# Optimization experiments

Measured on AMD Instinct MI355X. Metric: run time of the kernel, lower is better.

## Reference

```python
import jax, jax.numpy as jnp
import numpy as np
from jax import lax

K = 8  # diffusion channels
T = 3  # diffusion steps


def setup_inputs() -> dict:
    key = jax.random.key(0)
    k1, k2, k3 = jax.random.split(key, 3)
    x = jax.random.normal(k1, (16, 1, 512, 512), dtype=jnp.float32)
    # per-step conv weights [T, out=k, in=1, kh, kw] and biases [T, k]
    W = jax.random.normal(k2, (T, K, 1, 3, 3), dtype=jnp.float32) * 0.1
    b = jax.random.normal(k3, (T, K), dtype=jnp.float32) * 0.1
    return {"x": x, "W": W, "b": b}


def _g(d):
    # mode 1 edge-stopping function: exp(-|d| / (1 + d^2))
    return jnp.exp(-jnp.abs(d) / (1.0 + d * d))


def reference(x, W, b):
    in_x = x  # [N,1,H,W]
    for t in range(T):
        d1 = lax.conv_general_dilated(
            in_x, W[t], window_strides=(1, 1), padding="SAME",
            dimension_numbers=("NCHW", "OIHW", "NCHW"),
        ) + b[t][None, :, None, None]  # [N,K,H,W]
        features = _g(d1) * d1
        # squash_tensor: sum over the K channels, keep channel dim of 1
        in_x = in_x - jnp.sum(features, axis=1, keepdims=True) / K
    return in_x
```

## Files before the change

kernel.cpp:

```cpp
#include <hip/hip_runtime.h>

static constexpr int IMG  = 512;
static constexpr int TILE = 64;

template<int WR, int PS, bool TO_GLOBAL>
__device__ __forceinline__ void diffuse_step(
    const float* __restrict__ prev, float* __restrict__ cur,
    const float* __restrict__ Wt, const float* __restrict__ bt,
    int ty0, int tx0, int halo, int tid, float* __restrict__ gout)
{
    for (int idx = tid; idx < WR * WR; idx += 256) {
        const int r = idx / WR;
        const int c = idx - r * WR;
        const float* p = prev + r * PS + c;
        const float n0 = p[0],      n1 = p[1],      n2 = p[2];
        const float n3 = p[PS],     n4 = p[PS+1],   n5 = p[PS+2];
        const float n6 = p[2*PS],   n7 = p[2*PS+1], n8 = p[2*PS+2];
        float acc = 0.0f;
#pragma unroll
        for (int k = 0; k < 8; ++k) {
            const float* wk = Wt + 9 * k;
            float d = bt[k];
            d = fmaf(wk[0], n0, d);
            d = fmaf(wk[1], n1, d);
            d = fmaf(wk[2], n2, d);
            d = fmaf(wk[3], n3, d);
            d = fmaf(wk[4], n4, d);
            d = fmaf(wk[5], n5, d);
            d = fmaf(wk[6], n6, d);
            d = fmaf(wk[7], n7, d);
            d = fmaf(wk[8], n8, d);
            const float t    = fmaf(d, d, 1.0f);
            const float rinv = __builtin_amdgcn_rcpf(t);
            const float e    = __builtin_amdgcn_exp2f(
                                   -1.442695040888963f * __builtin_fabsf(d) * rinv);
            acc = fmaf(e, d, acc);
        }
        float v = n4 - acc * 0.125f;
        if (TO_GLOBAL) {
            const int gy = ty0 + r, gx = tx0 + c;
            gout[gy * IMG + gx] = v;
        } else {
            const int gy = ty0 - halo + r, gx = tx0 - halo + c;
            if (gy < 0 || gy >= IMG || gx < 0 || gx >= IMG) v = 0.0f;
            cur[r * WR + c] = v;
        }
    }
}

__global__ __launch_bounds__(256) void deep_ad_kernel(
    const float* __restrict__ x, const float* __restrict__ W,
    const float* __restrict__ b, float* __restrict__ out)
{
    __shared__ float A[70 * 70];
    __shared__ float Bs[68 * 68];

    const int tid = threadIdx.x;
    const int tx0 = blockIdx.x * TILE;
    const int ty0 = blockIdx.y * TILE;
    const float* xin  = x   + (size_t)blockIdx.z * (IMG * IMG);
    float*       gout = out + (size_t)blockIdx.z * (IMG * IMG);

    for (int idx = tid; idx < 70 * 70; idx += 256) {
        const int r = idx / 70, c = idx - (idx / 70) * 70;
        const int gy = ty0 + r - 3, gx = tx0 + c - 3;
        float v = 0.0f;
        if (gy >= 0 && gy < IMG && gx >= 0 && gx < IMG) v = xin[gy * IMG + gx];
        A[idx] = v;
    }
    __syncthreads();

    diffuse_step<68, 70, false>(A,  Bs, W + 0,   b + 0,  ty0, tx0, 2, tid, nullptr);
    __syncthreads();
    diffuse_step<66, 68, false>(Bs, A,  W + 72,  b + 8,  ty0, tx0, 1, tid, nullptr);
    __syncthreads();
    diffuse_step<64, 66, true >(A, nullptr, W + 144, b + 16, ty0, tx0, 0, tid, gout);
}

extern "C" void kernel_launch(void* const* d_in, const int* in_sizes, int n_in,
                              void* d_out, int out_size, void* d_ws, size_t ws_size,
                              hipStream_t stream)
{
    const float* x = (const float*)d_in[0];
    const float* W = (const float*)d_in[1];
    const float* b = (const float*)d_in[2];
    float* out = (float*)d_out;
    const int N = in_sizes[0] / (IMG * IMG);
    dim3 grid(IMG / TILE, IMG / TILE, N);
    deep_ad_kernel<<<grid, 256, 0, stream>>>(x, W, b, out);
}
```

Measured before the change: 128.4 us.

## Compute four pixels per thread with float4 LDS tiles and 64x32 blocks

```diff
diff --git a/kernel.cpp b/kernel.cpp
--- a/kernel.cpp
+++ b/kernel.cpp
@@ -1,80 +1,118 @@
 #include <hip/hip_runtime.h>
 
-static constexpr int IMG  = 512;
-static constexpr int TILE = 64;
+static constexpr int IMG = 512;
+static constexpr int TX  = 64;
+static constexpr int TY  = 32;
+static constexpr int LST = 72;
+static constexpr int SROWS = TY + 6;
 
-template<int WR, int PS, bool TO_GLOBAL>
+template<int WOFF, int NR, int RLO, int NG, bool TO_GLOBAL>
 __device__ __forceinline__ void diffuse_step(
     const float* __restrict__ prev, float* __restrict__ cur,
     const float* __restrict__ Wt, const float* __restrict__ bt,
-    int ty0, int tx0, int halo, int tid, float* __restrict__ gout)
+    int xoff , int ty0, int tx0,
+    int tid, float* __restrict__ gout)
 {
-    for (int idx = tid; idx < WR * WR; idx += 256) {
-        const int r = idx / WR;
-        const int c = idx - r * WR;
-        const float* p = prev + r * PS + c;
-        const float n0 = p[0],      n1 = p[1],      n2 = p[2];
-        const float n3 = p[PS],     n4 = p[PS+1],   n5 = p[PS+2];
-        const float n6 = p[2*PS],   n7 = p[2*PS+1], n8 = p[2*PS+2];
-        float acc = 0.0f;
+    constexpr int LOADW  = WOFF ? 8 : 6;
+    constexpr int NITEMS = NR * NG;
+    for (int idx = tid; idx < NITEMS; idx += 256) {
+        const int rr = idx / NG;
+        const int j  = idx - rr * NG;
+        const int r  = RLO + rr;
+        const int c0 = 4 * j;
+        const float* base = prev + (r - 1) * LST + c0;
+
+        float L0[LOADW], L1[LOADW], L2[LOADW];
+        *(float4*)&L0[0] = *(const float4*)(base);
+        *(float4*)&L1[0] = *(const float4*)(base + LST);
+        *(float4*)&L2[0] = *(const float4*)(base + 2 * LST);
+        if (WOFF) {
+            *(float4*)&L0[4] = *(const float4*)(base + 4);
+            *(float4*)&L1[4] = *(const float4*)(base + LST + 4);
+            *(float4*)&L2[4] = *(const float4*)(base + 2 * LST + 4);
+        } else {
+            *(float2*)&L0[4] = *(const float2*)(base + 4);
+            *(float2*)&L1[4] = *(const float2*)(base + LST + 4);
+            *(float2*)&L2[4] = *(const float2*)(base + 2 * LST + 4);
+        }
+
+        float acc[4] = {0.f, 0.f, 0.f, 0.f};
 #pragma unroll
         for (int k = 0; k < 8; ++k) {
-            const float* wk = Wt + 9 * k;
-            float d = bt[k];
-            d = fmaf(wk[0], n0, d);
-            d = fmaf(wk[1], n1, d);
-            d = fmaf(wk[2], n2, d);
-            d = fmaf(wk[3], n3, d);
-            d = fmaf(wk[4], n4, d);
-            d = fmaf(wk[5], n5, d);
-            d = fmaf(wk[6], n6, d);
-            d = fmaf(wk[7], n7, d);
-            d = fmaf(wk[8], n8, d);
-            const float t    = fmaf(d, d, 1.0f);
-            const float rinv = __builtin_amdgcn_rcpf(t);
-            const float e    = __builtin_amdgcn_exp2f(
-                                   -1.442695040888963f * __builtin_fabsf(d) * rinv);
-            acc = fmaf(e, d, acc);
+            const float w0 = Wt[9*k+0], w1 = Wt[9*k+1], w2 = Wt[9*k+2];
+            const float w3 = Wt[9*k+3], w4 = Wt[9*k+4], w5 = Wt[9*k+5];
+            const float w6 = Wt[9*k+6], w7 = Wt[9*k+7], w8 = Wt[9*k+8];
+            const float bk = bt[k];
+#pragma unroll
+            for (int i = 0; i < 4; ++i) {
+                float d = bk;
+                d = fmaf(w0, L0[WOFF+i],   d);
+                d = fmaf(w1, L0[WOFF+i+1], d);
+                d = fmaf(w2, L0[WOFF+i+2], d);
+                d = fmaf(w3, L1[WOFF+i],   d);
+                d = fmaf(w4, L1[WOFF+i+1], d);
+                d = fmaf(w5, L1[WOFF+i+2], d);
+                d = fmaf(w6, L2[WOFF+i],   d);
+                d = fmaf(w7, L2[WOFF+i+1], d);
+                d = fmaf(w8, L2[WOFF+i+2], d);
+                const float t    = fmaf(d, d, 1.0f);
+                const float rinv = __builtin_amdgcn_rcpf(t);
+                const float e    = __builtin_amdgcn_exp2f(
+                                       -1.442695040888963f * __builtin_fabsf(d) * rinv);
+                acc[i] = fmaf(e, d, acc[i]);
+            }
         }
-        float v = n4 - acc * 0.125f;
+
+        float4 v;
+        v.x = L1[WOFF+1] - acc[0] * 0.125f;
+        v.y = L1[WOFF+2] - acc[1] * 0.125f;
+        v.z = L1[WOFF+3] - acc[2] * 0.125f;
+        v.w = L1[WOFF+4] - acc[3] * 0.125f;
+
+        const int gy = ty0 - 3 + r;
         if (TO_GLOBAL) {
-            const int gy = ty0 + r, gx = tx0 + c;
-            gout[gy * IMG + gx] = v;
+            *(float4*)&gout[gy * IMG + tx0 + c0] = v;
         } else {
-            const int gy = ty0 - halo + r, gx = tx0 - halo + c;
-            if (gy < 0 || gy >= IMG || gx < 0 || gx >= IMG) v = 0.0f;
-            cur[r * WR + c] = v;
+            const bool ry  = (unsigned)gy < (unsigned)IMG;
+            const int  gx0 = xoff + c0;
+            v.x = (ry && (unsigned)(gx0 + 0) < (unsigned)IMG) ? v.x : 0.f;
+            v.y = (ry && (unsigned)(gx0 + 1) < (unsigned)IMG) ? v.y : 0.f;
+            v.z = (ry && (unsigned)(gx0 + 2) < (unsigned)IMG) ? v.z : 0.f;
+            v.w = (ry && (unsigned)(gx0 + 3) < (unsigned)IMG) ? v.w : 0.f;
+            *(float4*)&cur[r * LST + c0] = v;
         }
     }
 }
 
-__global__ __launch_bounds__(256) void deep_ad_kernel(
+__global__ __launch_bounds__(256, 6) void deep_ad_kernel(
     const float* __restrict__ x, const float* __restrict__ W,
     const float* __restrict__ b, float* __restrict__ out)
 {
-    __shared__ float A[70 * 70];
-    __shared__ float Bs[68 * 68];
+    __shared__ float A[SROWS * LST];
+    __shared__ float Bs[SROWS * LST];
 
     const int tid = threadIdx.x;
-    const int tx0 = blockIdx.x * TILE;
-    const int ty0 = blockIdx.y * TILE;
+    const int tx0 = blockIdx.x * TX;
+    const int ty0 = blockIdx.y * TY;
     const float* xin  = x   + (size_t)blockIdx.z * (IMG * IMG);
     float*       gout = out + (size_t)blockIdx.z * (IMG * IMG);
 
-    for (int idx = tid; idx < 70 * 70; idx += 256) {
-        const int r = idx / 70, c = idx - (idx / 70) * 70;
-        const int gy = ty0 + r - 3, gx = tx0 + c - 3;
-        float v = 0.0f;
-        if (gy >= 0 && gy < IMG && gx >= 0 && gx < IMG) v = xin[gy * IMG + gx];
-        A[idx] = v;
+    for (int idx = tid; idx < SROWS * 18; idx += 256) {
+        const int r = idx / 18, j = idx - (idx / 18) * 18;
+        const int gy = ty0 - 3 + r;
+        const int gx = tx0 - 4 + 4 * j;
+        float4 v = {0.f, 0.f, 0.f, 0.f};
+        if ((unsigned)gy < (unsigned)IMG && (unsigned)gx < (unsigned)IMG)
+            v = *(const float4*)(xin + gy * IMG + gx);
+        *(float4*)&A[r * LST + 4 * j] = v;
     }
     __syncthreads();
 
-    diffuse_step<68, 70, false>(A,  Bs, W + 0,   b + 0,  ty0, tx0, 2, tid, nullptr);
+    diffuse_step<1, TY + 4, 1, 17, false>(A,  Bs, W + 0,   b + 0,  tx0 - 2, ty0, tx0, tid, nullptr);
     __syncthreads();
-    diffuse_step<66, 68, false>(Bs, A,  W + 72,  b + 8,  ty0, tx0, 1, tid, nullptr);
+    diffuse_step<0, TY + 2, 2, 17, false>(Bs, A,  W + 72,  b + 8,  tx0 - 1, ty0, tx0, tid, nullptr);
     __syncthreads();
-    diffuse_step<64, 66, true >(A, nullptr, W + 144, b + 16, ty0, tx0, 0, tid, gout);
+    diffuse_step<0, TY,     3, 16, true >(A, nullptr, W + 144, b + 16, 0, ty0, tx0, tid, gout);
 }
 
 extern "C" void kernel_launch(void* const* d_in, const int* in_sizes, int n_in,
@@ -86,6 +124,6 @@
     const float* b = (const float*)d_in[2];
     float* out = (float*)d_out;
     const int N = in_sizes[0] / (IMG * IMG);
-    dim3 grid(IMG / TILE, IMG / TILE, N);
+    dim3 grid(IMG / TX, IMG / TY, N);
     deep_ad_kernel<<<grid, 256, 0, stream>>>(x, W, b, out);
 }
```

After: 130.7 us. About the same (+1.8%).
